# Optimization experiments

Hardware: AMD Instinct MI355X
Metric: run time of the kernel (lower is better)

Reference implementation:

```python
import jax, jax.numpy as jnp
import numpy as np

B, N, D = 32, 2048, 512
K = 64          # cluster_size
G = 16          # ghost_clusters
BN_EPS = 1e-5
L2_EPS = 1e-12


def setup_inputs() -> dict:
    key = jax.random.key(0)
    k1, k2, k3 = jax.random.split(key, 3)
    init_sc = 1.0 / np.sqrt(D)
    x = jax.random.normal(k1, (B, N, D), dtype=jnp.float32)
    clusters = init_sc * jax.random.normal(k2, (D, K + G), dtype=jnp.float32)
    clusters2 = init_sc * jax.random.normal(k3, (D, K), dtype=jnp.float32)
    bn_gamma = jnp.ones((K + G,), dtype=jnp.float32)
    bn_beta = jnp.zeros((K + G,), dtype=jnp.float32)
    return {"x": x, "clusters": clusters, "clusters2": clusters2,
            "bn_gamma": bn_gamma, "bn_beta": bn_beta}


def _l2norm(v, axis):
    n = jnp.sqrt(jnp.sum(v * v, axis=axis, keepdims=True))
    return v / jnp.maximum(n, L2_EPS)


def reference(x, clusters, clusters2, bn_gamma, bn_beta):
    b, n, d = x.shape
    kc = clusters2.shape[1]
    # projection: [B*N, K+G]
    a = x.reshape(-1, d) @ clusters
    # BatchNorm1d (training mode: batch statistics, biased variance)
    mean = jnp.mean(a, axis=0)
    var = jnp.mean((a - mean) ** 2, axis=0)
    a = (a - mean) * jax.lax.rsqrt(var + BN_EPS) * bn_gamma + bn_beta
    # softmax over all clusters, drop ghost clusters
    a = jax.nn.softmax(a, axis=1)[:, :kc].reshape(b, n, kc)
    # fused VLAD: v[b,d,k] = sum_n a[b,n,k] * (x[b,n,d] - c2[d,k])
    a_sum = jnp.sum(a, axis=1)                              # [B, K]
    vlad = jnp.einsum('bnd,bnk->bdk', x, a)                 # [B, D, K]
    vlad = vlad - clusters2[None, :, :] * a_sum[:, None, :]
    # intra-normalize over D, flatten, global L2 normalize
    vlad = _l2norm(vlad, axis=1)
    vlad = vlad.reshape(b, kc * d)
    vlad = _l2norm(vlad, axis=1)
    return vlad
```

## Files before the change

kernel.cpp:

```cpp
#include <hip/hip_runtime.h>
#include <hip/hip_bf16.h>

#define B_ 32
#define N_ 2048
#define D_ 512
#define KC_ 64
#define KG_ 80
#define M_ (B_*N_)

typedef __attribute__((ext_vector_type(8))) short short8;
typedef __attribute__((ext_vector_type(4))) float f32x4;

__device__ __forceinline__ unsigned short bf_rn(float f){
  unsigned int u = __float_as_uint(f);
  unsigned int r = u + 0x7FFFu + ((u >> 16) & 1u);
  return (unsigned short)(r >> 16);
}
__device__ __forceinline__ float bf_up(unsigned short h){
  return __uint_as_float(((unsigned int)h) << 16);
}
__device__ __forceinline__ void cvt8(const float* v, short8& hi, short8& lo){
#pragma unroll
  for (int i=0;i<8;i++){
    unsigned short h = bf_rn(v[i]);
    float rem = v[i] - bf_up(h);
    hi[i] = (short)h;
    lo[i] = (short)bf_rn(rem);
  }
}

__global__ __launch_bounds__(256) void k0_prep(const float* __restrict__ cl,
                                               unsigned short* __restrict__ Bf)
{
  int tid = blockIdx.x*256 + threadIdx.x;
  int l  = tid & 63;
  int hl = (tid >> 6) & 1;
  int j  = (tid >> 7) % 5;
  int c  = tid / 640;
  int kk  = c*32 + (l>>4)*8;
  int col = j*16 + (l&15);
  unsigned short o[8];
#pragma unroll
  for (int jj=0;jj<8;jj++){
    float v = cl[(size_t)(kk+jj)*KG_ + col];
    unsigned short h = bf_rn(v);
    if (hl == 0) o[jj] = h;
    else         o[jj] = bf_rn(v - bf_up(h));
  }
  size_t base = (size_t)c*5120 + (size_t)(j*2+hl)*512 + l*8;
#pragma unroll
  for (int jj=0;jj<8;jj++) Bf[base + jj] = o[jj];
}

__global__ __launch_bounds__(256) void k1_proj(
    const float* __restrict__ x, const unsigned short* __restrict__ Bf,
    float* __restrict__ a, float* __restrict__ S1, float* __restrict__ S2)
{
  __shared__ unsigned short Bs[2][5120];
  __shared__ float ls1[KG_], ls2[KG_];
  const int t = threadIdx.x;
  const int w = t >> 6, lane = t & 63;
  const int m = lane & 15, q = lane >> 4;
  const int rowW = blockIdx.x*128 + w*32;
  if (t < KG_){ ls1[t]=0.f; ls2[t]=0.f; }

  const float* xr0 = x + (size_t)(rowW + m)*D_ + q*8;
  const float* xr1 = xr0 + (size_t)16*D_;

  f32x4 acc[2][5];
#pragma unroll
  for (int rt=0;rt<2;rt++)
#pragma unroll
    for (int j=0;j<5;j++) acc[rt][j] = (f32x4){0.f,0.f,0.f,0.f};

  short8 sreg0, sreg1, sreg2;
  {
    const unsigned short* src = Bf;
    sreg0 = *(const short8*)(src + t*8);
    sreg1 = *(const short8*)(src + (256+t)*8);
    if (t < 128) sreg2 = *(const short8*)(src + (512+t)*8);
    *(short8*)&Bs[0][t*8] = sreg0;
    *(short8*)&Bs[0][(256+t)*8] = sreg1;
    if (t < 128) *(short8*)&Bs[0][(512+t)*8] = sreg2;
  }
  float v0[8], v1[8], nv0[8], nv1[8];
  *(float4*)&v0[0] = *(const float4*)(xr0);
  *(float4*)&v0[4] = *(const float4*)(xr0 + 4);
  *(float4*)&v1[0] = *(const float4*)(xr1);
  *(float4*)&v1[4] = *(const float4*)(xr1 + 4);
  __syncthreads();

  for (int c=0;c<16;c++){
    const int cur = c & 1;
    if (c < 15){
      const unsigned short* src = Bf + (size_t)(c+1)*5120;
      sreg0 = *(const short8*)(src + t*8);
      sreg1 = *(const short8*)(src + (256+t)*8);
      if (t < 128) sreg2 = *(const short8*)(src + (512+t)*8);
      *(float4*)&nv0[0] = *(const float4*)(xr0 + (c+1)*32);
      *(float4*)&nv0[4] = *(const float4*)(xr0 + (c+1)*32 + 4);
      *(float4*)&nv1[0] = *(const float4*)(xr1 + (c+1)*32);
      *(float4*)&nv1[4] = *(const float4*)(xr1 + (c+1)*32 + 4);
    }
    short8 ah0, al0, ah1, al1;
    cvt8(v0, ah0, al0);
    cvt8(v1, ah1, al1);
#pragma unroll
    for (int j=0;j<5;j++){
      short8 bh = *(const short8*)&Bs[cur][j*1024 + lane*8];
      short8 bl = *(const short8*)&Bs[cur][j*1024 + 512 + lane*8];
      acc[0][j] = __builtin_amdgcn_mfma_f32_16x16x32_bf16(ah0, bh, acc[0][j], 0,0,0);
      acc[0][j] = __builtin_amdgcn_mfma_f32_16x16x32_bf16(al0, bh, acc[0][j], 0,0,0);
      acc[0][j] = __builtin_amdgcn_mfma_f32_16x16x32_bf16(ah0, bl, acc[0][j], 0,0,0);
      acc[1][j] = __builtin_amdgcn_mfma_f32_16x16x32_bf16(ah1, bh, acc[1][j], 0,0,0);
      acc[1][j] = __builtin_amdgcn_mfma_f32_16x16x32_bf16(al1, bh, acc[1][j], 0,0,0);
      acc[1][j] = __builtin_amdgcn_mfma_f32_16x16x32_bf16(ah1, bl, acc[1][j], 0,0,0);
    }
    if (c < 15){
      const int nb = cur ^ 1;
      *(short8*)&Bs[nb][t*8] = sreg0;
      *(short8*)&Bs[nb][(256+t)*8] = sreg1;
      if (t < 128) *(short8*)&Bs[nb][(512+t)*8] = sreg2;
#pragma unroll
      for (int i=0;i<8;i++){ v0[i]=nv0[i]; v1[i]=nv1[i]; }
    }
    __syncthreads();
  }

  float s1v[5] = {0,0,0,0,0}, s2v[5] = {0,0,0,0,0};
#pragma unroll
  for (int rt=0;rt<2;rt++){
#pragma unroll
    for (int j=0;j<5;j++){
      f32x4 vv = acc[rt][j];
      size_t base = (size_t)(rowW + rt*16 + q*4)*KG_ + j*16 + m;
      a[base]        = vv[0];
      a[base+KG_]    = vv[1];
      a[base+2*KG_]  = vv[2];
      a[base+3*KG_]  = vv[3];
      s1v[j] += vv[0]+vv[1]+vv[2]+vv[3];
      s2v[j] += vv[0]*vv[0]+vv[1]*vv[1]+vv[2]*vv[2]+vv[3]*vv[3];
    }
  }
#pragma unroll
  for (int j=0;j<5;j++){
    float s1 = s1v[j], s2 = s2v[j];
    s1 += __shfl_xor(s1,16); s1 += __shfl_xor(s1,32);
    s2 += __shfl_xor(s2,16); s2 += __shfl_xor(s2,32);
    if (q == 0){
      atomicAdd(&ls1[j*16+m], s1);
      atomicAdd(&ls2[j*16+m], s2);
    }
  }
  __syncthreads();
  if (t < KG_){ atomicAdd(&S1[t], ls1[t]); atomicAdd(&S2[t], ls2[t]); }
}

__global__ void k2_bn(const float* __restrict__ S1, const float* __restrict__ S2,
                      const float* __restrict__ gamma, const float* __restrict__ beta,
                      float* __restrict__ scale, float* __restrict__ shift)
{
  int t = threadIdx.x;
  if (t < KG_){
    const float invM = 1.0f / (float)M_;
    float mean = S1[t] * invM;
    float var  = S2[t] * invM - mean*mean;
    float sc = gamma[t] * rsqrtf(var + 1e-5f);
    scale[t] = sc;
    shift[t] = beta[t] - mean*sc;
  }
}

__global__ __launch_bounds__(256) void k3_softmax(
    const float* __restrict__ a, const float* __restrict__ scale,
    const float* __restrict__ shift, float* __restrict__ asum,
    unsigned short* __restrict__ pth, unsigned short* __restrict__ ptl)
{
  __shared__ float as[64*84];
  __shared__ float sc[KG_], sh[KG_];
  __shared__ float lsum[KC_];
  const int t = threadIdx.x;
  const int row0 = blockIdx.x * 64;
  if (t < KG_){ sc[t]=scale[t]; sh[t]=shift[t]; }
  if (t < KC_) lsum[t]=0.f;
  __syncthreads();
#pragma unroll
  for (int l=0;l<20;l++){
    int idx = t + 256*l;
    int r = idx/80, col = idx - r*80;
    float v = a[(size_t)(row0+r)*KG_ + col];
    as[r*84+col] = v*sc[col] + sh[col];
  }
  __syncthreads();
  const int rt = t >> 2;
  const int g  = t & 3;
  float mx = -1e30f;
#pragma unroll
  for (int c=0;c<20;c++) mx = fmaxf(mx, as[rt*84 + g + 4*c]);
  mx = fmaxf(mx, __shfl_xor(mx,1));
  mx = fmaxf(mx, __shfl_xor(mx,2));
  float e[20]; float s = 0.f;
#pragma unroll
  for (int c=0;c<20;c++){ float v = __expf(as[rt*84 + g + 4*c] - mx); e[c]=v; s+=v; }
  s += __shfl_xor(s,1);
  s += __shfl_xor(s,2);
  const float inv = 1.f/s;
#pragma unroll
  for (int c=0;c<16;c++){
    int col = g + 4*c;
    float pv = e[c]*inv;
    as[rt*84 + col] = pv;
    float su = pv;
    su += __shfl_xor(su,4);  su += __shfl_xor(su,8);
    su += __shfl_xor(su,16); su += __shfl_xor(su,32);
    if ((t&63) < 4) atomicAdd(&lsum[col], su);
  }
  __syncthreads();
  {
    const int k = t >> 2, nseg = (t & 3) * 16;
    const int b = row0 >> 11, n0 = row0 & (N_-1);
    unsigned short vh[16], vl[16];
#pragma unroll
    for (int i=0;i<16;i++){
      float v = as[(nseg+i)*84 + k];
      unsigned short h = bf_rn(v);
      vh[i] = h;
      vl[i] = bf_rn(v - bf_up(h));
    }
    size_t base = ((size_t)b*KC_ + k)*N_ + n0 + nseg;
    *(short8*)&pth[base]     = *(short8*)&vh[0];
    *(short8*)&pth[base + 8] = *(short8*)&vh[8];
    *(short8*)&ptl[base]     = *(short8*)&vl[0];
    *(short8*)&ptl[base + 8] = *(short8*)&vl[8];
  }
  if (t < KC_) atomicAdd(&asum[(blockIdx.x>>5)*KC_ + t], lsum[t]);
}

__global__ __launch_bounds__(256) void k4_vlad(
    const float* __restrict__ x, const unsigned short* __restrict__ pth,
    const unsigned short* __restrict__ ptl, float* __restrict__ vp)
{
  __shared__ unsigned short xh[2][2560], xl[2][2560];
  const int t = threadIdx.x;
  const int blk = blockIdx.x;
  const int ns = blk & 3;
  const int dt = (blk >> 2) & 7;
  const int b  = blk >> 5;
  const int w = t >> 6, lane = t & 63;
  const int m = lane & 15, q = lane >> 4;
  const int d0 = dt*64;
  const int nbase = ns*512;
  const int dloc = t & 63, ng = t >> 6;

  const float* xbase = x + ((size_t)b*N_ + nbase)*D_ + d0 + dloc;
  const unsigned short* phb = pth + ((size_t)b*KC_ + m)*N_ + nbase + q*8;
  const unsigned short* plb = ptl + ((size_t)b*KC_ + m)*N_ + nbase + q*8;

  f32x4 acc[4];
#pragma unroll
  for (int j=0;j<4;j++) acc[j] = (f32x4){0.f,0.f,0.f,0.f};

  short8 pb[4][2], npb[4][2];
#pragma unroll
  for (int j=0;j<4;j++){
    pb[j][0] = *(const short8*)(phb + (size_t)(j*16)*N_);
    pb[j][1] = *(const short8*)(plb + (size_t)(j*16)*N_);
  }
  {
    float xv[8];
#pragma unroll
    for (int jj=0;jj<8;jj++) xv[jj] = xbase[(size_t)(ng*8+jj)*D_];
    short8 hi, lo; cvt8(xv, hi, lo);
    *(short8*)&xh[0][dloc*40 + ng*8] = hi;
    *(short8*)&xl[0][dloc*40 + ng*8] = lo;
  }
  __syncthreads();

  for (int ch=0; ch<16; ch++){
    const int cur = ch & 1;
    float nxv[8];
    if (ch < 15){
      const int no = (ch+1)*32;
#pragma unroll
      for (int jj=0;jj<8;jj++) nxv[jj] = xbase[(size_t)(no + ng*8+jj)*D_];
#pragma unroll
      for (int j=0;j<4;j++){
        npb[j][0] = *(const short8*)(phb + (size_t)(j*16)*N_ + no);
        npb[j][1] = *(const short8*)(plb + (size_t)(j*16)*N_ + no);
      }
    }
    short8 ahi = *(const short8*)&xh[cur][(w*16+m)*40 + q*8];
    short8 alo = *(const short8*)&xl[cur][(w*16+m)*40 + q*8];
#pragma unroll
    for (int j=0;j<4;j++){
      acc[j] = __builtin_amdgcn_mfma_f32_16x16x32_bf16(ahi, pb[j][0], acc[j], 0,0,0);
      acc[j] = __builtin_amdgcn_mfma_f32_16x16x32_bf16(alo, pb[j][0], acc[j], 0,0,0);
      acc[j] = __builtin_amdgcn_mfma_f32_16x16x32_bf16(ahi, pb[j][1], acc[j], 0,0,0);
    }
    if (ch < 15){
      short8 hi, lo; cvt8(nxv, hi, lo);
      *(short8*)&xh[cur^1][dloc*40 + ng*8] = hi;
      *(short8*)&xl[cur^1][dloc*40 + ng*8] = lo;
#pragma unroll
      for (int j=0;j<4;j++){ pb[j][0]=npb[j][0]; pb[j][1]=npb[j][1]; }
    }
    __syncthreads();
  }
#pragma unroll
  for (int j=0;j<4;j++){
    f32x4 v = acc[j];
    size_t base = (((size_t)ns*B_ + b)*D_ + d0 + w*16 + q*4)*KC_ + j*16 + m;
    vp[base]         = v[0];
    vp[base +   KC_] = v[1];
    vp[base + 2*KC_] = v[2];
    vp[base + 3*KC_] = v[3];
  }
}

__global__ __launch_bounds__(1024) void k5_norm(
    const float* __restrict__ vp, const float* __restrict__ c2,
    const float* __restrict__ asum, float* __restrict__ out)
{
  __shared__ float part[16][64];
  __shared__ float invd[64];
  __shared__ float gi_s;
  const int b = blockIdx.x;
  const int t = threadIdx.x;
  const int k = t & 63, dg = t >> 6;
  const float av = asum[b*KC_ + k];
  const size_t stride = (size_t)B_*D_*KC_;
  float v[32];
  float ss = 0.f;
#pragma unroll
  for (int s=0;s<32;s++){
    int d = dg + 16*s;
    size_t idx = ((size_t)b*D_ + d)*KC_ + k;
    float vv = 0.f;
#pragma unroll
    for (int nsp=0;nsp<4;nsp++) vv += vp[idx + (size_t)nsp*stride];
    vv -= c2[d*KC_ + k]*av;
    v[s] = vv;
    ss += vv*vv;
  }
  part[dg][k] = ss;
  __syncthreads();
  if (t < 64){
    float n2 = 0.f;
#pragma unroll
    for (int i=0;i<16;i++) n2 += part[i][t];
    float nn = sqrtf(n2);
    float denom = fmaxf(nn, 1e-12f);
    invd[t] = 1.f/denom;
    float ratio = nn/denom;
    float r2 = ratio*ratio;
#pragma unroll
    for (int mm=1;mm<64;mm<<=1) r2 += __shfl_xor(r2, mm);
    if (t==0){
      float g = sqrtf(r2);
      gi_s = 1.f/fmaxf(g, 1e-12f);
    }
  }
  __syncthreads();
  const float gi = gi_s;
  const float ik = invd[k];
#pragma unroll
  for (int s=0;s<32;s++){
    int d = dg + 16*s;
    out[(size_t)b*(D_*KC_) + (size_t)d*KC_ + k] = v[s]*ik*gi;
  }
}

extern "C" void kernel_launch(void* const* d_in, const int* in_sizes, int n_in,
                              void* d_out, int out_size, void* d_ws, size_t ws_size,
                              hipStream_t stream)
{
  const float* x     = (const float*)d_in[0];
  const float* cl    = (const float*)d_in[1];
  const float* c2    = (const float*)d_in[2];
  const float* gamma = (const float*)d_in[3];
  const float* beta  = (const float*)d_in[4];
  float* out = (float*)d_out;
  float* ws  = (float*)d_ws;

  float* S1    = ws;
  float* S2    = ws + 80;
  float* scale = ws + 160;
  float* shift = ws + 240;
  float* asum  = ws + 320;
  unsigned short* Bf = (unsigned short*)(ws + 4096);
  float* a     = ws + 45056;
  unsigned short* pth = (unsigned short*)(ws + 5287936);
  unsigned short* ptl = (unsigned short*)(ws + 7385088);
  float* vp    = a;

  hipMemsetAsync(ws, 0, 2368*sizeof(float), stream);
  k0_prep   <<<40,   256, 0, stream>>>(cl, Bf);
  k1_proj   <<<512,  256, 0, stream>>>(x, Bf, a, S1, S2);
  k2_bn     <<<1,    128, 0, stream>>>(S1, S2, gamma, beta, scale, shift);
  k3_softmax<<<1024, 256, 0, stream>>>(a, scale, shift, asum, pth, ptl);
  k4_vlad   <<<1024, 256, 0, stream>>>(x, pth, ptl, vp);
  k5_norm   <<<32,  1024, 0, stream>>>(vp, c2, asum, out);
}
```

Baseline: 310.7 us.

## Emit transposed bf16 x from projection kernel and drop LDS staging in VLAD

The projection kernel now writes a transposed bf16 (hi-only) copy of x while it converts it. The VLAD kernel reads that copy directly from global memory instead of re-reading fp32 x with strided loads and staging through LDS. The projection also drops LDS staging of the cluster matrix, loading B fragments straight into registers, and uses one row-tile per wave across twice as many blocks. VLAD now keeps only the hi part of x, cutting one MFMA per step at some cost in precision, and the scattered 2-byte transposed stores add write traffic.

```diff
diff --git a/kernel.cpp b/kernel.cpp
--- a/kernel.cpp
+++ b/kernel.cpp
@@ -52,95 +52,82 @@
   for (int jj=0;jj<8;jj++) Bf[base + jj] = o[jj];
 }
 
-__global__ __launch_bounds__(256) void k1_proj(
+__global__ __launch_bounds__(256,3) void k1_proj(
     const float* __restrict__ x, const unsigned short* __restrict__ Bf,
-    float* __restrict__ a, float* __restrict__ S1, float* __restrict__ S2)
-{
-  __shared__ unsigned short Bs[2][5120];
+    float* __restrict__ a, float* __restrict__ S1, float* __restrict__ S2,
+    unsigned short* __restrict__ xth)
+{
   __shared__ float ls1[KG_], ls2[KG_];
   const int t = threadIdx.x;
   const int w = t >> 6, lane = t & 63;
   const int m = lane & 15, q = lane >> 4;
-  const int rowW = blockIdx.x*128 + w*32;
+  const int row = blockIdx.x*64 + w*16 + m;
+  const int gb = row >> 11, nn = row & (N_-1);
   if (t < KG_){ ls1[t]=0.f; ls2[t]=0.f; }
-
-  const float* xr0 = x + (size_t)(rowW + m)*D_ + q*8;
-  const float* xr1 = xr0 + (size_t)16*D_;
-
-  f32x4 acc[2][5];
-#pragma unroll
-  for (int rt=0;rt<2;rt++)
-#pragma unroll
-    for (int j=0;j<5;j++) acc[rt][j] = (f32x4){0.f,0.f,0.f,0.f};
-
-  short8 sreg0, sreg1, sreg2;
+  __syncthreads();
+
+  const float* xr = x + (size_t)row*D_ + q*8;
+
+  f32x4 acc[5];
+#pragma unroll
+  for (int j=0;j<5;j++) acc[j] = (f32x4){0.f,0.f,0.f,0.f};
+
+  float4 va0 = *(const float4*)(xr);
+  float4 vb0 = *(const float4*)(xr + 4);
+  float4 va1 = *(const float4*)(xr + 32);
+  float4 vb1 = *(const float4*)(xr + 36);
+  short8 bf[10];
   {
-    const unsigned short* src = Bf;
-    sreg0 = *(const short8*)(src + t*8);
-    sreg1 = *(const short8*)(src + (256+t)*8);
-    if (t < 128) sreg2 = *(const short8*)(src + (512+t)*8);
-    *(short8*)&Bs[0][t*8] = sreg0;
-    *(short8*)&Bs[0][(256+t)*8] = sreg1;
-    if (t < 128) *(short8*)&Bs[0][(512+t)*8] = sreg2;
-  }
-  float v0[8], v1[8], nv0[8], nv1[8];
-  *(float4*)&v0[0] = *(const float4*)(xr0);
-  *(float4*)&v0[4] = *(const float4*)(xr0 + 4);
-  *(float4*)&v1[0] = *(const float4*)(xr1);
-  *(float4*)&v1[4] = *(const float4*)(xr1 + 4);
-  __syncthreads();
+    const unsigned short* bp = Bf + lane*8;
+#pragma unroll
+    for (int f=0; f<10; f++) bf[f] = *(const short8*)(bp + f*512);
+  }
 
   for (int c=0;c<16;c++){
-    const int cur = c & 1;
+    float4 va2, vb2;
+    if (c < 14){
+      va2 = *(const float4*)(xr + (c+2)*32);
+      vb2 = *(const float4*)(xr + (c+2)*32 + 4);
+    }
+    short8 nbf[10];
     if (c < 15){
-      const unsigned short* src = Bf + (size_t)(c+1)*5120;
-      sreg0 = *(const short8*)(src + t*8);
-      sreg1 = *(const short8*)(src + (256+t)*8);
-      if (t < 128) sreg2 = *(const short8*)(src + (512+t)*8);
-      *(float4*)&nv0[0] = *(const float4*)(xr0 + (c+1)*32);
-      *(float4*)&nv0[4] = *(const float4*)(xr0 + (c+1)*32 + 4);
-      *(float4*)&nv1[0] = *(const float4*)(xr1 + (c+1)*32);
-      *(float4*)&nv1[4] = *(const float4*)(xr1 + (c+1)*32 + 4);
-    }
-    short8 ah0, al0, ah1, al1;
-    cvt8(v0, ah0, al0);
-    cvt8(v1, ah1, al1);
+      const unsigned short* np = Bf + (size_t)(c+1)*5120 + lane*8;
+#pragma unroll
+      for (int f=0; f<10; f++) nbf[f] = *(const short8*)(np + f*512);
+    }
+    float v[8] = {va0.x,va0.y,va0.z,va0.w,vb0.x,vb0.y,vb0.z,vb0.w};
+    short8 ah, al;
+    cvt8(v, ah, al);
+    {
+      size_t xo = ((size_t)gb*D_ + c*32 + q*8)*N_ + nn;
+#pragma unroll
+      for (int j=0;j<8;j++) xth[xo + (size_t)j*N_] = (unsigned short)ah[j];
+    }
 #pragma unroll
     for (int j=0;j<5;j++){
-      short8 bh = *(const short8*)&Bs[cur][j*1024 + lane*8];
-      short8 bl = *(const short8*)&Bs[cur][j*1024 + 512 + lane*8];
-      acc[0][j] = __builtin_amdgcn_mfma_f32_16x16x32_bf16(ah0, bh, acc[0][j], 0,0,0);
-      acc[0][j] = __builtin_amdgcn_mfma_f32_16x16x32_bf16(al0, bh, acc[0][j], 0,0,0);
-      acc[0][j] = __builtin_amdgcn_mfma_f32_16x16x32_bf16(ah0, bl, acc[0][j], 0,0,0);
-      acc[1][j] = __builtin_amdgcn_mfma_f32_16x16x32_bf16(ah1, bh, acc[1][j], 0,0,0);
-      acc[1][j] = __builtin_amdgcn_mfma_f32_16x16x32_bf16(al1, bh, acc[1][j], 0,0,0);
-      acc[1][j] = __builtin_amdgcn_mfma_f32_16x16x32_bf16(ah1, bl, acc[1][j], 0,0,0);
-    }
+      acc[j] = __builtin_amdgcn_mfma_f32_16x16x32_bf16(ah, bf[2*j],   acc[j], 0,0,0);
+      acc[j] = __builtin_amdgcn_mfma_f32_16x16x32_bf16(al, bf[2*j],   acc[j], 0,0,0);
+      acc[j] = __builtin_amdgcn_mfma_f32_16x16x32_bf16(ah, bf[2*j+1], acc[j], 0,0,0);
+    }
+    va0 = va1; vb0 = vb1; va1 = va2; vb1 = vb2;
     if (c < 15){
-      const int nb = cur ^ 1;
-      *(short8*)&Bs[nb][t*8] = sreg0;
-      *(short8*)&Bs[nb][(256+t)*8] = sreg1;
-      if (t < 128) *(short8*)&Bs[nb][(512+t)*8] = sreg2;
-#pragma unroll
-      for (int i=0;i<8;i++){ v0[i]=nv0[i]; v1[i]=nv1[i]; }
-    }
-    __syncthreads();
-  }
-
-  float s1v[5] = {0,0,0,0,0}, s2v[5] = {0,0,0,0,0};
-#pragma unroll
-  for (int rt=0;rt<2;rt++){
-#pragma unroll
-    for (int j=0;j<5;j++){
-      f32x4 vv = acc[rt][j];
-      size_t base = (size_t)(rowW + rt*16 + q*4)*KG_ + j*16 + m;
-      a[base]        = vv[0];
-      a[base+KG_]    = vv[1];
-      a[base+2*KG_]  = vv[2];
-      a[base+3*KG_]  = vv[3];
-      s1v[j] += vv[0]+vv[1]+vv[2]+vv[3];
-      s2v[j] += vv[0]*vv[0]+vv[1]*vv[1]+vv[2]*vv[2]+vv[3]*vv[3];
-    }
+#pragma unroll
+      for (int f=0; f<10; f++) bf[f] = nbf[f];
+    }
+  }
+
+  const int rowbase = blockIdx.x*64 + w*16;
+  float s1v[5], s2v[5];
+#pragma unroll
+  for (int j=0;j<5;j++){
+    f32x4 vv = acc[j];
+    size_t base = (size_t)(rowbase + q*4)*KG_ + j*16 + m;
+    a[base]        = vv[0];
+    a[base+KG_]    = vv[1];
+    a[base+2*KG_]  = vv[2];
+    a[base+3*KG_]  = vv[3];
+    s1v[j] = vv[0]+vv[1]+vv[2]+vv[3];
+    s2v[j] = vv[0]*vv[0]+vv[1]*vv[1]+vv[2]*vv[2]+vv[3]*vv[3];
   }
 #pragma unroll
   for (int j=0;j<5;j++){
@@ -236,84 +223,60 @@
   if (t < KC_) atomicAdd(&asum[(blockIdx.x>>5)*KC_ + t], lsum[t]);
 }
 
-__global__ __launch_bounds__(256) void k4_vlad(
-    const float* __restrict__ x, const unsigned short* __restrict__ pth,
+__global__ __launch_bounds__(256,4) void k4_vlad(
+    const unsigned short* __restrict__ xth, const unsigned short* __restrict__ pth,
     const unsigned short* __restrict__ ptl, float* __restrict__ vp)
 {
-  __shared__ unsigned short xh[2][2560], xl[2][2560];
   const int t = threadIdx.x;
-  const int blk = blockIdx.x;
-  const int ns = blk & 3;
-  const int dt = (blk >> 2) & 7;
-  const int b  = blk >> 5;
   const int w = t >> 6, lane = t & 63;
   const int m = lane & 15, q = lane >> 4;
-  const int d0 = dt*64;
-  const int nbase = ns*512;
-  const int dloc = t & 63, ng = t >> 6;
-
-  const float* xbase = x + ((size_t)b*N_ + nbase)*D_ + d0 + dloc;
-  const unsigned short* phb = pth + ((size_t)b*KC_ + m)*N_ + nbase + q*8;
-  const unsigned short* plb = ptl + ((size_t)b*KC_ + m)*N_ + nbase + q*8;
+  const int blk = blockIdx.x;
+  const int dt = blk >> 7;
+  const int b  = (blk >> 2) & 31;
+  const int ns = blk & 3;
+
+  const unsigned short* ap  = pth + ((size_t)b*KC_ + w*16 + m)*N_ + ns*512 + q*8;
+  const unsigned short* lp  = ptl + ((size_t)b*KC_ + w*16 + m)*N_ + ns*512 + q*8;
+  const unsigned short* bpx = xth + ((size_t)b*D_ + dt*64 + m)*N_ + ns*512 + q*8;
 
   f32x4 acc[4];
 #pragma unroll
   for (int j=0;j<4;j++) acc[j] = (f32x4){0.f,0.f,0.f,0.f};
 
-  short8 pb[4][2], npb[4][2];
-#pragma unroll
-  for (int j=0;j<4;j++){
-    pb[j][0] = *(const short8*)(phb + (size_t)(j*16)*N_);
-    pb[j][1] = *(const short8*)(plb + (size_t)(j*16)*N_);
-  }
-  {
-    float xv[8];
-#pragma unroll
-    for (int jj=0;jj<8;jj++) xv[jj] = xbase[(size_t)(ng*8+jj)*D_];
-    short8 hi, lo; cvt8(xv, hi, lo);
-    *(short8*)&xh[0][dloc*40 + ng*8] = hi;
-    *(short8*)&xl[0][dloc*40 + ng*8] = lo;
-  }
-  __syncthreads();
+  short8 pa = *(const short8*)ap;
+  short8 pl = *(const short8*)lp;
+  short8 xb[4];
+#pragma unroll
+  for (int j=0;j<4;j++) xb[j] = *(const short8*)(bpx + (size_t)(j*16)*N_);
 
   for (int ch=0; ch<16; ch++){
-    const int cur = ch & 1;
-    float nxv[8];
+    short8 npa, npl, nxb[4];
     if (ch < 15){
       const int no = (ch+1)*32;
-#pragma unroll
-      for (int jj=0;jj<8;jj++) nxv[jj] = xbase[(size_t)(no + ng*8+jj)*D_];
-#pragma unroll
-      for (int j=0;j<4;j++){
-        npb[j][0] = *(const short8*)(phb + (size_t)(j*16)*N_ + no);
-        npb[j][1] = *(const short8*)(plb + (size_t)(j*16)*N_ + no);
-      }
-    }
-    short8 ahi = *(const short8*)&xh[cur][(w*16+m)*40 + q*8];
-    short8 alo = *(const short8*)&xl[cur][(w*16+m)*40 + q*8];
+      npa = *(const short8*)(ap + no);
+      npl = *(const short8*)(lp + no);
+#pragma unroll
+      for (int j=0;j<4;j++) nxb[j] = *(const short8*)(bpx + (size_t)(j*16)*N_ + no);
+    }
 #pragma unroll
     for (int j=0;j<4;j++){
-      acc[j] = __builtin_amdgcn_mfma_f32_16x16x32_bf16(ahi, pb[j][0], acc[j], 0,0,0);
-      acc[j] = __builtin_amdgcn_mfma_f32_16x16x32_bf16(alo, pb[j][0], acc[j], 0,0,0);
-      acc[j] = __builtin_amdgcn_mfma_f32_16x16x32_bf16(ahi, pb[j][1], acc[j], 0,0,0);
+      acc[j] = __builtin_amdgcn_mfma_f32_16x16x32_bf16(pa, xb[j], acc[j], 0,0,0);
+      acc[j] = __builtin_amdgcn_mfma_f32_16x16x32_bf16(pl, xb[j], acc[j], 0,0,0);
     }
     if (ch < 15){
-      short8 hi, lo; cvt8(nxv, hi, lo);
-      *(short8*)&xh[cur^1][dloc*40 + ng*8] = hi;
-      *(short8*)&xl[cur^1][dloc*40 + ng*8] = lo;
-#pragma unroll
-      for (int j=0;j<4;j++){ pb[j][0]=npb[j][0]; pb[j][1]=npb[j][1]; }
-    }
-    __syncthreads();
+      pa = npa; pl = npl;
+#pragma unroll
+      for (int j=0;j<4;j++) xb[j] = nxb[j];
+    }
   }
 #pragma unroll
   for (int j=0;j<4;j++){
-    f32x4 v = acc[j];
-    size_t base = (((size_t)ns*B_ + b)*D_ + d0 + w*16 + q*4)*KC_ + j*16 + m;
-    vp[base]         = v[0];
-    vp[base +   KC_] = v[1];
-    vp[base + 2*KC_] = v[2];
-    vp[base + 3*KC_] = v[3];
+#pragma unroll
+    for (int i=0;i<4;i++){
+      int k = w*16 + q*4 + i;
+      int d = dt*64 + j*16 + m;
+      vp[(((size_t)ns*B_ + b)*D_ + d)*KC_ + k] = acc[j][i];
+    }
   }
 }
 
@@ -387,17 +350,18 @@
   float* scale = ws + 160;
   float* shift = ws + 240;
   float* asum  = ws + 320;
-  unsigned short* Bf = (unsigned short*)(ws + 4096);
+  unsigned short* Bf  = (unsigned short*)(ws + 4096);
   float* a     = ws + 45056;
   unsigned short* pth = (unsigned short*)(ws + 5287936);
   unsigned short* ptl = (unsigned short*)(ws + 7385088);
+  unsigned short* xth = (unsigned short*)(ws + 9482240);
   float* vp    = a;
 
   hipMemsetAsync(ws, 0, 2368*sizeof(float), stream);
   k0_prep   <<<40,   256, 0, stream>>>(cl, Bf);
-  k1_proj   <<<512,  256, 0, stream>>>(x, Bf, a, S1, S2);
+  k1_proj   <<<1024, 256, 0, stream>>>(x, Bf, a, S1, S2, xth);
   k2_bn     <<<1,    128, 0, stream>>>(S1, S2, gamma, beta, scale, shift);
   k3_softmax<<<1024, 256, 0, stream>>>(a, scale, shift, asum, pth, ptl);
-  k4_vlad   <<<1024, 256, 0, stream>>>(x, pth, ptl, vp);
+  k4_vlad   <<<1024, 256, 0, stream>>>(xth, pth, ptl, vp);
   k5_norm   <<<32,  1024, 0, stream>>>(vp, c2, asum, out);
 }
```

After: 326.2 us. 5.0% more time.
